# Kernel tuning notes

Measured on AMD Instinct MI355X. Metric: run time of the kernel, lower is better.

The kernel has to match this reference:

```python
import jax, jax.numpy as jnp
import numpy as np

N = 50000
E = 800000
D_IN, D_HID, D_OUT = 256, 512, 256
LN_EPS = 1e-5


def setup_inputs() -> dict:
    key = jax.random.key(0)
    ks = jax.random.split(key, 8)
    return {
        "v": jax.random.normal(ks[0], (N, D_IN), dtype=jnp.float32),
        "edge_weight": jax.random.uniform(ks[1], (E,), dtype=jnp.float32),
        "epsilon": jnp.zeros((1, 1), dtype=jnp.float32),
        "w1": jax.random.normal(ks[2], (D_HID, D_IN), dtype=jnp.float32) * (1.0 / np.sqrt(D_IN)),
        "b1": jnp.zeros((D_HID,), dtype=jnp.float32),
        "g1": jnp.ones((D_HID,), dtype=jnp.float32),
        "beta1": jnp.zeros((D_HID,), dtype=jnp.float32),
        "w2": jax.random.normal(ks[3], (D_OUT, D_HID), dtype=jnp.float32) * (1.0 / np.sqrt(D_HID)),
        "b2": jnp.zeros((D_OUT,), dtype=jnp.float32),
        "g2": jnp.ones((D_OUT,), dtype=jnp.float32),
        "beta2": jnp.zeros((D_OUT,), dtype=jnp.float32),
        "src": jax.random.randint(ks[4], (E,), 0, N, dtype=jnp.int32),
        "dst": jax.random.randint(ks[5], (E,), 0, N, dtype=jnp.int32),
    }


def _layer_norm(x, g, b):
    mu = jnp.mean(x, axis=-1, keepdims=True)
    var = jnp.mean(jnp.square(x - mu), axis=-1, keepdims=True)
    return (x - mu) * jax.lax.rsqrt(var + LN_EPS) * g + b


def reference(v, edge_weight, epsilon, w1, b1, g1, beta1, w2, b2, g2, beta2, src, dst):
    # sparse adjacency aggregation: agg[dst] += w * v[src]   (torch.sparse.mm(a, v))
    msgs = v[src] * edge_weight[:, None]            # [E, D_IN]
    agg = jax.ops.segment_sum(msgs, dst, num_segments=v.shape[0])  # [N, D_IN]
    h = agg + epsilon * v                            # epsilon residual
    # MLP: Linear -> LayerNorm -> ReLU  (x2)
    h = jax.nn.relu(_layer_norm(h @ w1.T + b1, g1, beta1))
    h = jax.nn.relu(_layer_norm(h @ w2.T + b2, g2, beta2))
    return h
```

## Files before the change

### kernel.cpp

```cpp
#include <hip/hip_runtime.h>

#define D_IN 256
#define D_HID 512
#define D_OUT 256
#define LN_EPS 1e-5f
#define SCAN_B 512

typedef __attribute__((ext_vector_type(8))) short bf16x8;
typedef __attribute__((ext_vector_type(4))) float f32x4;

__device__ __forceinline__ ushort f2bf(float x) {
    union { float f; unsigned u; } c; c.f = x;
    unsigned r = c.u + 0x7FFFu + ((c.u >> 16) & 1u);
    return (ushort)(r >> 16);
}
__device__ __forceinline__ float bf2f(unsigned b) {
    union { unsigned u; float f; } c; c.u = b << 16;
    return c.f;
}

__global__ void prep_kernel(const float* __restrict__ v, const float* __restrict__ w1,
                            const float* __restrict__ w2, ushort* __restrict__ vb,
                            ushort* __restrict__ w1p, ushort* __restrict__ w2p,
                            const int* __restrict__ dst, int* __restrict__ rank,
                            int* __restrict__ cnt, int n4v, int E,
                            int bv, int bw) {
    int b = blockIdx.x, t = threadIdx.x;
    if (b < bv) {
        int i = b * 256 + t;
        if (i < n4v) {
            float4 x = ((const float4*)v)[i];
            ((ushort4*)vb)[i] = make_ushort4(f2bf(x.x), f2bf(x.y), f2bf(x.z), f2bf(x.w));
        }
    } else if (b < bv + bw) {
        int j = (b - bv) * 256 + t;
        if (j < 32768) {
            int f = j * 4;
            int row = f >> 8, col = f & 255;
            float4 x = ((const float4*)w1)[j];
            int rb = row >> 4, fr = row & 15;
            int kb32 = col >> 5, q = (col & 31) >> 3, e = col & 7;
            int chunk = (kb32 * 32 + rb) * 64 + q * 16 + fr;
            *(ushort4*)(w1p + chunk * 8 + e) =
                make_ushort4(f2bf(x.x), f2bf(x.y), f2bf(x.z), f2bf(x.w));
        } else {
            int k = j - 32768;
            int f = k * 4;
            int row = f >> 9, col = f & 511;
            float4 x = ((const float4*)w2)[k];
            int rb = row >> 4, fr = row & 15;
            int kb32 = col >> 5, q = (col & 31) >> 3, e = col & 7;
            int chunk = (kb32 * 16 + rb) * 64 + q * 16 + fr;
            *(ushort4*)(w2p + chunk * 8 + e) =
                make_ushort4(f2bf(x.x), f2bf(x.y), f2bf(x.z), f2bf(x.w));
        }
    } else {
        int e = (b - bv - bw) * 256 + t;
        if (e < E) rank[e] = atomicAdd(&cnt[dst[e]], 1);
    }
}

__global__ __launch_bounds__(SCAN_B) void scan1_kernel(const int* __restrict__ cnt,
                                                       int* __restrict__ offs,
                                                       int* __restrict__ bsum, int n) {
    __shared__ int s[SCAN_B];
    int i = blockIdx.x * SCAN_B + threadIdx.x;
    int x = (i < n) ? cnt[i] : 0;
    s[threadIdx.x] = x;
    __syncthreads();
    for (int o = 1; o < SCAN_B; o <<= 1) {
        int t = (threadIdx.x >= (unsigned)o) ? s[threadIdx.x - o] : 0;
        __syncthreads();
        s[threadIdx.x] += t;
        __syncthreads();
    }
    if (i < n) offs[i] = s[threadIdx.x] - x;
    if (threadIdx.x == SCAN_B - 1) bsum[blockIdx.x] = s[threadIdx.x];
}

__global__ __launch_bounds__(SCAN_B) void scan3_kernel(int* __restrict__ offs,
                                                       const int* __restrict__ bsum,
                                                       int n, int E, int nb) {
    __shared__ int s[SCAN_B];
    int t = threadIdx.x;
    s[t] = (t < nb && t < (int)blockIdx.x) ? bsum[t] : 0;
    __syncthreads();
    for (int o = SCAN_B / 2; o > 0; o >>= 1) {
        if (t < o) s[t] += s[t + o];
        __syncthreads();
    }
    int base = s[0];
    int i = blockIdx.x * SCAN_B + t;
    if (i < n) offs[i] += base;
    if (i == 0) offs[n] = E;
}

__global__ void fill_kernel(const int* __restrict__ src, const int* __restrict__ dst,
                            const float* __restrict__ ew, const int* __restrict__ rank,
                            const int* __restrict__ offs,
                            int2* __restrict__ perm, int E) {
    int e = blockIdx.x * 256 + threadIdx.x;
    if (e >= E) return;
    int p = offs[dst[e]] + rank[e];
    perm[p] = make_int2(src[e], __float_as_int(ew[e]));
}

__global__ __launch_bounds__(256) void aggregate_kernel(
    const ushort* __restrict__ vb, const float* __restrict__ eps_p,
    const int* __restrict__ offs, const int2* __restrict__ perm,
    ushort* __restrict__ aggb, int N) {
    int node = blockIdx.x * 4 + (threadIdx.x >> 6);
    if (node >= N) return;
    int lane = threadIdx.x & 63;
    int beg = offs[node], end = offs[node + 1];
    float a0 = 0.f, a1 = 0.f, a2 = 0.f, a3 = 0.f;
    float c0 = 0.f, c1 = 0.f, c2 = 0.f, c3 = 0.f;

    int i = beg;
    for (; i + 8 <= end; i += 8) {
        int2 p0 = perm[i + 0], p1 = perm[i + 1], p2 = perm[i + 2], p3 = perm[i + 3];
        int2 p4 = perm[i + 4], p5 = perm[i + 5], p6 = perm[i + 6], p7 = perm[i + 7];
        float w0 = __int_as_float(p0.y), w1 = __int_as_float(p1.y);
        float w2 = __int_as_float(p2.y), w3 = __int_as_float(p3.y);
        float w4 = __int_as_float(p4.y), w5 = __int_as_float(p5.y);
        float w6 = __int_as_float(p6.y), w7 = __int_as_float(p7.y);
        ushort4 r0 = ((const ushort4*)(vb + (size_t)p0.x * D_IN))[lane];
        ushort4 r1 = ((const ushort4*)(vb + (size_t)p1.x * D_IN))[lane];
        ushort4 r2 = ((const ushort4*)(vb + (size_t)p2.x * D_IN))[lane];
        ushort4 r3 = ((const ushort4*)(vb + (size_t)p3.x * D_IN))[lane];
        ushort4 r4 = ((const ushort4*)(vb + (size_t)p4.x * D_IN))[lane];
        ushort4 r5 = ((const ushort4*)(vb + (size_t)p5.x * D_IN))[lane];
        ushort4 r6 = ((const ushort4*)(vb + (size_t)p6.x * D_IN))[lane];
        ushort4 r7 = ((const ushort4*)(vb + (size_t)p7.x * D_IN))[lane];
        a0 += w0 * bf2f(r0.x) + w1 * bf2f(r1.x) + w2 * bf2f(r2.x) + w3 * bf2f(r3.x);
        a1 += w0 * bf2f(r0.y) + w1 * bf2f(r1.y) + w2 * bf2f(r2.y) + w3 * bf2f(r3.y);
        a2 += w0 * bf2f(r0.z) + w1 * bf2f(r1.z) + w2 * bf2f(r2.z) + w3 * bf2f(r3.z);
        a3 += w0 * bf2f(r0.w) + w1 * bf2f(r1.w) + w2 * bf2f(r2.w) + w3 * bf2f(r3.w);
        c0 += w4 * bf2f(r4.x) + w5 * bf2f(r5.x) + w6 * bf2f(r6.x) + w7 * bf2f(r7.x);
        c1 += w4 * bf2f(r4.y) + w5 * bf2f(r5.y) + w6 * bf2f(r6.y) + w7 * bf2f(r7.y);
        c2 += w4 * bf2f(r4.z) + w5 * bf2f(r5.z) + w6 * bf2f(r6.z) + w7 * bf2f(r7.z);
        c3 += w4 * bf2f(r4.w) + w5 * bf2f(r5.w) + w6 * bf2f(r6.w) + w7 * bf2f(r7.w);
    }
    for (; i + 4 <= end; i += 4) {
        int2 p0 = perm[i + 0], p1 = perm[i + 1], p2 = perm[i + 2], p3 = perm[i + 3];
        float w0 = __int_as_float(p0.y), w1 = __int_as_float(p1.y);
        float w2 = __int_as_float(p2.y), w3 = __int_as_float(p3.y);
        ushort4 r0 = ((const ushort4*)(vb + (size_t)p0.x * D_IN))[lane];
        ushort4 r1 = ((const ushort4*)(vb + (size_t)p1.x * D_IN))[lane];
        ushort4 r2 = ((const ushort4*)(vb + (size_t)p2.x * D_IN))[lane];
        ushort4 r3 = ((const ushort4*)(vb + (size_t)p3.x * D_IN))[lane];
        a0 += w0 * bf2f(r0.x) + w1 * bf2f(r1.x) + w2 * bf2f(r2.x) + w3 * bf2f(r3.x);
        a1 += w0 * bf2f(r0.y) + w1 * bf2f(r1.y) + w2 * bf2f(r2.y) + w3 * bf2f(r3.y);
        a2 += w0 * bf2f(r0.z) + w1 * bf2f(r1.z) + w2 * bf2f(r2.z) + w3 * bf2f(r3.z);
        a3 += w0 * bf2f(r0.w) + w1 * bf2f(r1.w) + w2 * bf2f(r2.w) + w3 * bf2f(r3.w);
    }
    for (; i < end; ++i) {
        int2 p = perm[i];
        float w = __int_as_float(p.y);
        ushort4 r = ((const ushort4*)(vb + (size_t)p.x * D_IN))[lane];
        a0 += w * bf2f(r.x); a1 += w * bf2f(r.y);
        a2 += w * bf2f(r.z); a3 += w * bf2f(r.w);
    }
    a0 += c0; a1 += c1; a2 += c2; a3 += c3;
    float eps = eps_p[0];
    ushort4 m = ((const ushort4*)(vb + (size_t)node * D_IN))[lane];
    a0 += eps * bf2f(m.x); a1 += eps * bf2f(m.y);
    a2 += eps * bf2f(m.z); a3 += eps * bf2f(m.w);
    ((ushort4*)(aggb + (size_t)node * D_IN))[lane] =
        make_ushort4(f2bf(a0), f2bf(a1), f2bf(a2), f2bf(a3));
}

#define HS_IDX(row, col) ((row) * 512 + ((col) ^ (((row) & 7) << 3)))
#define AT_IDX(row, col) ((row) * 256 + ((col) ^ (((row) & 7) << 3)))

__global__ __launch_bounds__(256, 2) void mlp_kernel(
    const ushort* __restrict__ A, const ushort* __restrict__ w1p,
    const ushort* __restrict__ w2p,
    const float* __restrict__ b1, const float* __restrict__ g1, const float* __restrict__ be1,
    const float* __restrict__ b2, const float* __restrict__ g2, const float* __restrict__ be2,
    float* __restrict__ out, int N) {
    __shared__ ushort hs[32768];
    __shared__ float redf[640];

    int t = threadIdx.x;
    int w = t >> 6, lane = t & 63;
    int row0 = blockIdx.x * 64;
    int fr = lane & 15, q = lane >> 4, kb = q * 8;

    #pragma unroll
    for (int j = 0; j < 8; ++j) {
        int p = (w * 8 + j) * 64 + lane;
        int row = p >> 5, cbs = p & 31;
        int colblk = cbs ^ (row & 7);
        int ar = row0 + row; if (ar > N - 1) ar = N - 1;
        const ushort* gp = A + (size_t)ar * D_IN + colblk * 8;
        __builtin_amdgcn_global_load_lds(
            (const __attribute__((address_space(1))) void*)gp,
            (__attribute__((address_space(3))) void*)(&hs[(w * 8 + j) * 512]),
            16, 0, 0);
    }

    bf16x8 bfb[2][8];
    #pragma unroll
    for (int c = 0; c < 8; ++c)
        bfb[0][c] = *(const bf16x8*)(w1p + (size_t)((0 * 32 + w * 8 + c) * 64 + lane) * 8);

    __syncthreads();

    f32x4 acc[4][8];
    #pragma unroll
    for (int m = 0; m < 4; ++m)
        #pragma unroll
        for (int c = 0; c < 8; ++c) {
            f32x4 z = {0.f, 0.f, 0.f, 0.f};
            acc[m][c] = z;
        }

    #pragma unroll
    for (int ks = 0; ks < 8; ++ks) {
        const int cur = ks & 1, nxt = cur ^ 1;
        if (ks < 7) {
            #pragma unroll
            for (int c = 0; c < 8; ++c)
                bfb[nxt][c] = *(const bf16x8*)(w1p +
                    (size_t)(((ks + 1) * 32 + w * 8 + c) * 64 + lane) * 8);
        }
        bf16x8 af[4];
        #pragma unroll
        for (int m = 0; m < 4; ++m)
            af[m] = *(const bf16x8*)&hs[AT_IDX(m * 16 + fr, ks * 32 + kb)];
        #pragma unroll
        for (int m = 0; m < 4; ++m)
            #pragma unroll
            for (int c = 0; c < 8; ++c)
                acc[m][c] = __builtin_amdgcn_mfma_f32_16x16x32_bf16(af[m], bfb[cur][c], acc[m][c], 0, 0, 0);
    }

    {
        float bi[8], gg[8], bb[8];
        #pragma unroll
        for (int c = 0; c < 8; ++c) {
            int col = w * 128 + c * 16 + fr;
            bi[c] = b1[col]; gg[c] = g1[col]; bb[c] = be1[col];
        }
        #pragma unroll
        for (int m = 0; m < 4; ++m) {
            #pragma unroll
            for (int r = 0; r < 4; ++r) {
                float s = 0.f, sq = 0.f;
                #pragma unroll
                for (int c = 0; c < 8; ++c) {
                    float x = acc[m][c][r] + bi[c];
                    acc[m][c][r] = x;
                    s += x; sq += x * x;
                }
                #pragma unroll
                for (int o = 1; o < 16; o <<= 1) {
                    s  += __shfl_xor(s, o, 64);
                    sq += __shfl_xor(sq, o, 64);
                }
                if (fr == 0) {
                    int row = m * 16 + q * 4 + r;
                    redf[row * 4 + w]       = s;
                    redf[256 + row * 4 + w] = sq;
                }
            }
        }
        __syncthreads();
        if (t < 64) {
            float s  = redf[t * 4 + 0] + redf[t * 4 + 1] + redf[t * 4 + 2] + redf[t * 4 + 3];
            float sq = redf[256 + t * 4 + 0] + redf[256 + t * 4 + 1] +
                       redf[256 + t * 4 + 2] + redf[256 + t * 4 + 3];
            float mu = s / (float)D_HID;
            float var = sq / (float)D_HID - mu * mu;
            redf[512 + t] = mu;
            redf[576 + t] = rsqrtf(var + LN_EPS);
        }
        __syncthreads();
        #pragma unroll
        for (int m = 0; m < 4; ++m) {
            #pragma unroll
            for (int r = 0; r < 4; ++r) {
                int row = m * 16 + q * 4 + r;
                float mu = redf[512 + row], rs = redf[576 + row];
                #pragma unroll
                for (int c = 0; c < 8; ++c) {
                    int col = w * 128 + c * 16 + fr;
                    float y = (acc[m][c][r] - mu) * rs * gg[c] + bb[c];
                    hs[HS_IDX(row, col)] = f2bf(fmaxf(y, 0.f));
                }
            }
        }
    }

    bf16x8 bf2b[2][4][2];
    #pragma unroll
    for (int c = 0; c < 4; ++c)
        #pragma unroll
        for (int h = 0; h < 2; ++h)
            bf2b[0][c][h] = *(const bf16x8*)(w2p +
                (size_t)(((0 + h) * 16 + w * 4 + c) * 64 + lane) * 8);

    __syncthreads();

    f32x4 acc2[4][4];
    #pragma unroll
    for (int m = 0; m < 4; ++m)
        #pragma unroll
        for (int c = 0; c < 4; ++c) {
            f32x4 z = {0.f, 0.f, 0.f, 0.f};
            acc2[m][c] = z;
        }

    #pragma unroll
    for (int s = 0; s < 8; ++s) {
        const int cur = s & 1, nxt = cur ^ 1;
        if (s < 7) {
            #pragma unroll
            for (int c = 0; c < 4; ++c)
                #pragma unroll
                for (int h = 0; h < 2; ++h)
                    bf2b[nxt][c][h] = *(const bf16x8*)(w2p +
                        (size_t)(((2 * (s + 1) + h) * 16 + w * 4 + c) * 64 + lane) * 8);
        }
        bf16x8 af2[4][2];
        #pragma unroll
        for (int m = 0; m < 4; ++m)
            #pragma unroll
            for (int h = 0; h < 2; ++h)
                af2[m][h] = *(const bf16x8*)&hs[HS_IDX(m * 16 + fr, s * 64 + h * 32 + kb)];
        #pragma unroll
        for (int m = 0; m < 4; ++m)
            #pragma unroll
            for (int c = 0; c < 4; ++c)
                #pragma unroll
                for (int h = 0; h < 2; ++h)
                    acc2[m][c] = __builtin_amdgcn_mfma_f32_16x16x32_bf16(af2[m][h], bf2b[cur][c][h], acc2[m][c], 0, 0, 0);
    }

    {
        float bi[4], gg[4], bb[4];
        #pragma unroll
        for (int c = 0; c < 4; ++c) {
            int col = w * 64 + c * 16 + fr;
            bi[c] = b2[col]; gg[c] = g2[col]; bb[c] = be2[col];
        }
        #pragma unroll
        for (int m = 0; m < 4; ++m) {
            #pragma unroll
            for (int r = 0; r < 4; ++r) {
                float s = 0.f, sq = 0.f;
                #pragma unroll
                for (int c = 0; c < 4; ++c) {
                    float x = acc2[m][c][r] + bi[c];
                    acc2[m][c][r] = x;
                    s += x; sq += x * x;
                }
                #pragma unroll
                for (int o = 1; o < 16; o <<= 1) {
                    s  += __shfl_xor(s, o, 64);
                    sq += __shfl_xor(sq, o, 64);
                }
                if (fr == 0) {
                    int row = m * 16 + q * 4 + r;
                    redf[row * 4 + w]       = s;
                    redf[256 + row * 4 + w] = sq;
                }
            }
        }
        __syncthreads();
        if (t < 64) {
            float s  = redf[t * 4 + 0] + redf[t * 4 + 1] + redf[t * 4 + 2] + redf[t * 4 + 3];
            float sq = redf[256 + t * 4 + 0] + redf[256 + t * 4 + 1] +
                       redf[256 + t * 4 + 2] + redf[256 + t * 4 + 3];
            float mu = s / (float)D_OUT;
            float var = sq / (float)D_OUT - mu * mu;
            redf[512 + t] = mu;
            redf[576 + t] = rsqrtf(var + LN_EPS);
        }
        __syncthreads();
        #pragma unroll
        for (int m = 0; m < 4; ++m) {
            #pragma unroll
            for (int r = 0; r < 4; ++r) {
                int row = m * 16 + q * 4 + r;
                int grow = row0 + row;
                if (grow >= N) continue;
                float mu = redf[512 + row], rs = redf[576 + row];
                #pragma unroll
                for (int c = 0; c < 4; ++c) {
                    int col = w * 64 + c * 16 + fr;
                    float y = (acc2[m][c][r] - mu) * rs * gg[c] + bb[c];
                    out[(size_t)grow * D_OUT + col] = fmaxf(y, 0.f);
                }
            }
        }
    }
}

extern "C" void kernel_launch(void* const* d_in, const int* in_sizes, int n_in,
                              void* d_out, int out_size, void* d_ws, size_t ws_size,
                              hipStream_t stream) {
    const float* v     = (const float*)d_in[0];
    const float* ew    = (const float*)d_in[1];
    const float* eps   = (const float*)d_in[2];
    const float* w1    = (const float*)d_in[3];
    const float* b1    = (const float*)d_in[4];
    const float* g1    = (const float*)d_in[5];
    const float* beta1 = (const float*)d_in[6];
    const float* w2    = (const float*)d_in[7];
    const float* b2    = (const float*)d_in[8];
    const float* g2    = (const float*)d_in[9];
    const float* beta2 = (const float*)d_in[10];
    const int*   src   = (const int*)d_in[11];
    const int*   dst   = (const int*)d_in[12];

    int N = in_sizes[0] / D_IN;
    int E = in_sizes[1];

    float* out = (float*)d_out;

    char* ws = (char*)d_ws;
    size_t off = 0;
    ushort* vb   = (ushort*)(ws + off); off += (size_t)N * D_IN * 2;
    ushort* aggb = (ushort*)(ws + off); off += (size_t)N * D_IN * 2;
    ushort* w1p  = (ushort*)(ws + off); off += (size_t)D_HID * D_IN * 2;
    ushort* w2p  = (ushort*)(ws + off); off += (size_t)D_OUT * D_HID * 2;
    int* offs     = (int*)(ws + off); off += (size_t)(N + 256) * 4;
    int* cnt      = (int*)(ws + off); off += (size_t)(N + 256) * 4;
    int* bsum     = (int*)(ws + off); off += 1024;
    int* rank     = (int*)(ws + off); off += (size_t)E * 4;
    int2* perm    = (int2*)(ws + off); off += (size_t)E * 8;

    int nb = (N + SCAN_B - 1) / SCAN_B;
    int n4v = N * (D_IN / 4);
    int bv = (n4v + 255) / 256;
    int bw = 256;
    int be = (E + 255) / 256;

    hipMemsetAsync(cnt, 0, (size_t)N * 4, stream);

    prep_kernel<<<bv + bw + be, 256, 0, stream>>>(v, w1, w2, vb, w1p, w2p,
                                                  dst, rank, cnt, n4v, E, bv, bw);

    scan1_kernel<<<nb, SCAN_B, 0, stream>>>(cnt, offs, bsum, N);
    scan3_kernel<<<nb, SCAN_B, 0, stream>>>(offs, bsum, N, E, nb);

    fill_kernel<<<be, 256, 0, stream>>>(src, dst, ew, rank, offs, perm, E);

    aggregate_kernel<<<(N + 3) / 4, 256, 0, stream>>>(vb, eps, offs, perm, aggb, N);

    int mblocks = (N + 63) / 64;
    mlp_kernel<<<mblocks, 256, 0, stream>>>(aggb, w1p, w2p,
                                            b1, g1, beta1, b2, g2, beta2, out, N);
}
```

Measured before the change: 294.7 us.

## Fuse preprocessing, scan, fill and aggregation into one persistent kernel with grid barriers

Replaces the prep, two scan, fill and aggregate launches with a single persistent kernel of fixed grid size that uses atomic-counter grid barriers between phases. The scan is restructured into 256-element chunks plus a single-block scan of chunk sums, and the base offsets are applied lazily when reading. The aim is to remove several kernel launch gaps and tail effects. In exchange, grid-stride loops run at lower occupancy, and the software barriers rely on all 960 blocks being co-resident, which risks deadlock if they are not.

```diff
diff --git a/kernel.cpp b/kernel.cpp
--- a/kernel.cpp
+++ b/kernel.cpp
@@ -4,7 +4,8 @@
 #define D_HID 512
 #define D_OUT 256
 #define LN_EPS 1e-5f
-#define SCAN_B 512
+#define NBLK 960
+#define NTHR (NBLK * 256)
 
 typedef __attribute__((ext_vector_type(8))) short bf16x8;
 typedef __attribute__((ext_vector_type(4))) float f32x4;
@@ -19,21 +20,35 @@
     return c.f;
 }
 
-__global__ void prep_kernel(const float* __restrict__ v, const float* __restrict__ w1,
-                            const float* __restrict__ w2, ushort* __restrict__ vb,
-                            ushort* __restrict__ w1p, ushort* __restrict__ w2p,
-                            const int* __restrict__ dst, int* __restrict__ rank,
-                            int* __restrict__ cnt, int n4v, int E,
-                            int bv, int bw) {
-    int b = blockIdx.x, t = threadIdx.x;
-    if (b < bv) {
-        int i = b * 256 + t;
-        if (i < n4v) {
-            float4 x = ((const float4*)v)[i];
-            ((ushort4*)vb)[i] = make_ushort4(f2bf(x.x), f2bf(x.y), f2bf(x.z), f2bf(x.w));
-        }
-    } else if (b < bv + bw) {
-        int j = (b - bv) * 256 + t;
+__device__ __forceinline__ void gbar(int* bar, int k) {
+    __threadfence();
+    __syncthreads();
+    if (threadIdx.x == 0) {
+        atomicAdd(&bar[k], 1);
+        while (atomicAdd(&bar[k], 0) < NBLK) __builtin_amdgcn_s_sleep(2);
+    }
+    __syncthreads();
+    __threadfence();
+}
+
+__global__ __launch_bounds__(256, 4) void mega_kernel(
+    const float* __restrict__ v, const float* __restrict__ w1,
+    const float* __restrict__ w2, ushort* __restrict__ vb,
+    ushort* __restrict__ w1p, ushort* __restrict__ w2p,
+    const int* __restrict__ src, const int* __restrict__ dst,
+    const float* __restrict__ ew, const float* __restrict__ eps_p,
+    int* __restrict__ rank, int* __restrict__ cnt, int* __restrict__ bar,
+    int* __restrict__ offs, int* __restrict__ bsum, int2* __restrict__ perm,
+    ushort* __restrict__ aggb, int N, int E, int n4v, int nch) {
+    __shared__ int s[256];
+    int t = threadIdx.x, b = blockIdx.x;
+    int tid = b * 256 + t;
+
+    for (int i = tid; i < n4v; i += NTHR) {
+        float4 x = ((const float4*)v)[i];
+        ((ushort4*)vb)[i] = make_ushort4(f2bf(x.x), f2bf(x.y), f2bf(x.z), f2bf(x.w));
+    }
+    for (int j = tid; j < 65536; j += NTHR) {
         if (j < 32768) {
             int f = j * 4;
             int row = f >> 8, col = f & 255;
@@ -54,120 +69,113 @@
             *(ushort4*)(w2p + chunk * 8 + e) =
                 make_ushort4(f2bf(x.x), f2bf(x.y), f2bf(x.z), f2bf(x.w));
         }
-    } else {
-        int e = (b - bv - bw) * 256 + t;
-        if (e < E) rank[e] = atomicAdd(&cnt[dst[e]], 1);
-    }
-}
-
-__global__ __launch_bounds__(SCAN_B) void scan1_kernel(const int* __restrict__ cnt,
-                                                       int* __restrict__ offs,
-                                                       int* __restrict__ bsum, int n) {
-    __shared__ int s[SCAN_B];
-    int i = blockIdx.x * SCAN_B + threadIdx.x;
-    int x = (i < n) ? cnt[i] : 0;
-    s[threadIdx.x] = x;
-    __syncthreads();
-    for (int o = 1; o < SCAN_B; o <<= 1) {
-        int t = (threadIdx.x >= (unsigned)o) ? s[threadIdx.x - o] : 0;
-        __syncthreads();
-        s[threadIdx.x] += t;
-        __syncthreads();
-    }
-    if (i < n) offs[i] = s[threadIdx.x] - x;
-    if (threadIdx.x == SCAN_B - 1) bsum[blockIdx.x] = s[threadIdx.x];
-}
-
-__global__ __launch_bounds__(SCAN_B) void scan3_kernel(int* __restrict__ offs,
-                                                       const int* __restrict__ bsum,
-                                                       int n, int E, int nb) {
-    __shared__ int s[SCAN_B];
-    int t = threadIdx.x;
-    s[t] = (t < nb && t < (int)blockIdx.x) ? bsum[t] : 0;
-    __syncthreads();
-    for (int o = SCAN_B / 2; o > 0; o >>= 1) {
-        if (t < o) s[t] += s[t + o];
-        __syncthreads();
-    }
-    int base = s[0];
-    int i = blockIdx.x * SCAN_B + t;
-    if (i < n) offs[i] += base;
-    if (i == 0) offs[n] = E;
-}
-
-__global__ void fill_kernel(const int* __restrict__ src, const int* __restrict__ dst,
-                            const float* __restrict__ ew, const int* __restrict__ rank,
-                            const int* __restrict__ offs,
-                            int2* __restrict__ perm, int E) {
-    int e = blockIdx.x * 256 + threadIdx.x;
-    if (e >= E) return;
-    int p = offs[dst[e]] + rank[e];
-    perm[p] = make_int2(src[e], __float_as_int(ew[e]));
-}
-
-__global__ __launch_bounds__(256) void aggregate_kernel(
-    const ushort* __restrict__ vb, const float* __restrict__ eps_p,
-    const int* __restrict__ offs, const int2* __restrict__ perm,
-    ushort* __restrict__ aggb, int N) {
-    int node = blockIdx.x * 4 + (threadIdx.x >> 6);
-    if (node >= N) return;
-    int lane = threadIdx.x & 63;
-    int beg = offs[node], end = offs[node + 1];
-    float a0 = 0.f, a1 = 0.f, a2 = 0.f, a3 = 0.f;
-    float c0 = 0.f, c1 = 0.f, c2 = 0.f, c3 = 0.f;
-
-    int i = beg;
-    for (; i + 8 <= end; i += 8) {
-        int2 p0 = perm[i + 0], p1 = perm[i + 1], p2 = perm[i + 2], p3 = perm[i + 3];
-        int2 p4 = perm[i + 4], p5 = perm[i + 5], p6 = perm[i + 6], p7 = perm[i + 7];
-        float w0 = __int_as_float(p0.y), w1 = __int_as_float(p1.y);
-        float w2 = __int_as_float(p2.y), w3 = __int_as_float(p3.y);
-        float w4 = __int_as_float(p4.y), w5 = __int_as_float(p5.y);
-        float w6 = __int_as_float(p6.y), w7 = __int_as_float(p7.y);
-        ushort4 r0 = ((const ushort4*)(vb + (size_t)p0.x * D_IN))[lane];
-        ushort4 r1 = ((const ushort4*)(vb + (size_t)p1.x * D_IN))[lane];
-        ushort4 r2 = ((const ushort4*)(vb + (size_t)p2.x * D_IN))[lane];
-        ushort4 r3 = ((const ushort4*)(vb + (size_t)p3.x * D_IN))[lane];
-        ushort4 r4 = ((const ushort4*)(vb + (size_t)p4.x * D_IN))[lane];
-        ushort4 r5 = ((const ushort4*)(vb + (size_t)p5.x * D_IN))[lane];
-        ushort4 r6 = ((const ushort4*)(vb + (size_t)p6.x * D_IN))[lane];
-        ushort4 r7 = ((const ushort4*)(vb + (size_t)p7.x * D_IN))[lane];
-        a0 += w0 * bf2f(r0.x) + w1 * bf2f(r1.x) + w2 * bf2f(r2.x) + w3 * bf2f(r3.x);
-        a1 += w0 * bf2f(r0.y) + w1 * bf2f(r1.y) + w2 * bf2f(r2.y) + w3 * bf2f(r3.y);
-        a2 += w0 * bf2f(r0.z) + w1 * bf2f(r1.z) + w2 * bf2f(r2.z) + w3 * bf2f(r3.z);
-        a3 += w0 * bf2f(r0.w) + w1 * bf2f(r1.w) + w2 * bf2f(r2.w) + w3 * bf2f(r3.w);
-        c0 += w4 * bf2f(r4.x) + w5 * bf2f(r5.x) + w6 * bf2f(r6.x) + w7 * bf2f(r7.x);
-        c1 += w4 * bf2f(r4.y) + w5 * bf2f(r5.y) + w6 * bf2f(r6.y) + w7 * bf2f(r7.y);
-        c2 += w4 * bf2f(r4.z) + w5 * bf2f(r5.z) + w6 * bf2f(r6.z) + w7 * bf2f(r7.z);
-        c3 += w4 * bf2f(r4.w) + w5 * bf2f(r5.w) + w6 * bf2f(r6.w) + w7 * bf2f(r7.w);
-    }
-    for (; i + 4 <= end; i += 4) {
-        int2 p0 = perm[i + 0], p1 = perm[i + 1], p2 = perm[i + 2], p3 = perm[i + 3];
-        float w0 = __int_as_float(p0.y), w1 = __int_as_float(p1.y);
-        float w2 = __int_as_float(p2.y), w3 = __int_as_float(p3.y);
-        ushort4 r0 = ((const ushort4*)(vb + (size_t)p0.x * D_IN))[lane];
-        ushort4 r1 = ((const ushort4*)(vb + (size_t)p1.x * D_IN))[lane];
-        ushort4 r2 = ((const ushort4*)(vb + (size_t)p2.x * D_IN))[lane];
-        ushort4 r3 = ((const ushort4*)(vb + (size_t)p3.x * D_IN))[lane];
-        a0 += w0 * bf2f(r0.x) + w1 * bf2f(r1.x) + w2 * bf2f(r2.x) + w3 * bf2f(r3.x);
-        a1 += w0 * bf2f(r0.y) + w1 * bf2f(r1.y) + w2 * bf2f(r2.y) + w3 * bf2f(r3.y);
-        a2 += w0 * bf2f(r0.z) + w1 * bf2f(r1.z) + w2 * bf2f(r2.z) + w3 * bf2f(r3.z);
-        a3 += w0 * bf2f(r0.w) + w1 * bf2f(r1.w) + w2 * bf2f(r2.w) + w3 * bf2f(r3.w);
-    }
-    for (; i < end; ++i) {
-        int2 p = perm[i];
-        float w = __int_as_float(p.y);
-        ushort4 r = ((const ushort4*)(vb + (size_t)p.x * D_IN))[lane];
-        a0 += w * bf2f(r.x); a1 += w * bf2f(r.y);
-        a2 += w * bf2f(r.z); a3 += w * bf2f(r.w);
-    }
-    a0 += c0; a1 += c1; a2 += c2; a3 += c3;
-    float eps = eps_p[0];
-    ushort4 m = ((const ushort4*)(vb + (size_t)node * D_IN))[lane];
-    a0 += eps * bf2f(m.x); a1 += eps * bf2f(m.y);
-    a2 += eps * bf2f(m.z); a3 += eps * bf2f(m.w);
-    ((ushort4*)(aggb + (size_t)node * D_IN))[lane] =
-        make_ushort4(f2bf(a0), f2bf(a1), f2bf(a2), f2bf(a3));
+    }
+    for (int e = tid; e < E; e += NTHR)
+        rank[e] = atomicAdd(&cnt[dst[e]], 1);
+
+    gbar(bar, 0);
+
+    if (b < nch) {
+        int i = b * 256 + t;
+        int x = cnt[i];
+        s[t] = x;
+        __syncthreads();
+        for (int o = 1; o < 256; o <<= 1) {
+            int u = (t >= o) ? s[t - o] : 0;
+            __syncthreads();
+            s[t] += u;
+            __syncthreads();
+        }
+        offs[i] = s[t] - x;
+        if (t == 255) bsum[b] = s[t];
+    }
+    gbar(bar, 1);
+
+    if (b == 0) {
+        int x = (t < nch) ? bsum[t] : 0;
+        s[t] = x;
+        __syncthreads();
+        for (int o = 1; o < 256; o <<= 1) {
+            int u = (t >= o) ? s[t - o] : 0;
+            __syncthreads();
+            s[t] += u;
+            __syncthreads();
+        }
+        bsum[t] = s[t] - x;
+    }
+    gbar(bar, 2);
+
+    for (int e = tid; e < E; e += NTHR) {
+        int d = dst[e];
+        int p = bsum[d >> 8] + offs[d] + rank[e];
+        perm[p] = make_int2(src[e], __float_as_int(ew[e]));
+    }
+    gbar(bar, 3);
+
+    {
+        const float eps = eps_p[0];
+        int lane = t & 63;
+        int wid = b * 4 + (t >> 6);
+        for (int node = wid; node < N; node += NBLK * 4) {
+            int beg = bsum[node >> 8] + offs[node];
+            int m = node + 1;
+            int end = (m < nch * 256) ? (bsum[m >> 8] + offs[m]) : E;
+            float a0 = 0.f, a1 = 0.f, a2 = 0.f, a3 = 0.f;
+            float c0 = 0.f, c1 = 0.f, c2 = 0.f, c3 = 0.f;
+
+            int i = beg;
+            for (; i + 8 <= end; i += 8) {
+                int2 p0 = perm[i + 0], p1 = perm[i + 1], p2 = perm[i + 2], p3 = perm[i + 3];
+                int2 p4 = perm[i + 4], p5 = perm[i + 5], p6 = perm[i + 6], p7 = perm[i + 7];
+                float w0 = __int_as_float(p0.y), w1_ = __int_as_float(p1.y);
+                float w2_ = __int_as_float(p2.y), w3 = __int_as_float(p3.y);
+                float w4 = __int_as_float(p4.y), w5 = __int_as_float(p5.y);
+                float w6 = __int_as_float(p6.y), w7 = __int_as_float(p7.y);
+                ushort4 r0 = ((const ushort4*)(vb + (size_t)p0.x * D_IN))[lane];
+                ushort4 r1 = ((const ushort4*)(vb + (size_t)p1.x * D_IN))[lane];
+                ushort4 r2 = ((const ushort4*)(vb + (size_t)p2.x * D_IN))[lane];
+                ushort4 r3 = ((const ushort4*)(vb + (size_t)p3.x * D_IN))[lane];
+                ushort4 r4 = ((const ushort4*)(vb + (size_t)p4.x * D_IN))[lane];
+                ushort4 r5 = ((const ushort4*)(vb + (size_t)p5.x * D_IN))[lane];
+                ushort4 r6 = ((const ushort4*)(vb + (size_t)p6.x * D_IN))[lane];
+                ushort4 r7 = ((const ushort4*)(vb + (size_t)p7.x * D_IN))[lane];
+                a0 += w0 * bf2f(r0.x) + w1_ * bf2f(r1.x) + w2_ * bf2f(r2.x) + w3 * bf2f(r3.x);
+                a1 += w0 * bf2f(r0.y) + w1_ * bf2f(r1.y) + w2_ * bf2f(r2.y) + w3 * bf2f(r3.y);
+                a2 += w0 * bf2f(r0.z) + w1_ * bf2f(r1.z) + w2_ * bf2f(r2.z) + w3 * bf2f(r3.z);
+                a3 += w0 * bf2f(r0.w) + w1_ * bf2f(r1.w) + w2_ * bf2f(r2.w) + w3 * bf2f(r3.w);
+                c0 += w4 * bf2f(r4.x) + w5 * bf2f(r5.x) + w6 * bf2f(r6.x) + w7 * bf2f(r7.x);
+                c1 += w4 * bf2f(r4.y) + w5 * bf2f(r5.y) + w6 * bf2f(r6.y) + w7 * bf2f(r7.y);
+                c2 += w4 * bf2f(r4.z) + w5 * bf2f(r5.z) + w6 * bf2f(r6.z) + w7 * bf2f(r7.z);
+                c3 += w4 * bf2f(r4.w) + w5 * bf2f(r5.w) + w6 * bf2f(r6.w) + w7 * bf2f(r7.w);
+            }
+            for (; i + 4 <= end; i += 4) {
+                int2 p0 = perm[i + 0], p1 = perm[i + 1], p2 = perm[i + 2], p3 = perm[i + 3];
+                float w0 = __int_as_float(p0.y), w1_ = __int_as_float(p1.y);
+                float w2_ = __int_as_float(p2.y), w3 = __int_as_float(p3.y);
+                ushort4 r0 = ((const ushort4*)(vb + (size_t)p0.x * D_IN))[lane];
+                ushort4 r1 = ((const ushort4*)(vb + (size_t)p1.x * D_IN))[lane];
+                ushort4 r2 = ((const ushort4*)(vb + (size_t)p2.x * D_IN))[lane];
+                ushort4 r3 = ((const ushort4*)(vb + (size_t)p3.x * D_IN))[lane];
+                a0 += w0 * bf2f(r0.x) + w1_ * bf2f(r1.x) + w2_ * bf2f(r2.x) + w3 * bf2f(r3.x);
+                a1 += w0 * bf2f(r0.y) + w1_ * bf2f(r1.y) + w2_ * bf2f(r2.y) + w3 * bf2f(r3.y);
+                a2 += w0 * bf2f(r0.z) + w1_ * bf2f(r1.z) + w2_ * bf2f(r2.z) + w3 * bf2f(r3.z);
+                a3 += w0 * bf2f(r0.w) + w1_ * bf2f(r1.w) + w2_ * bf2f(r2.w) + w3 * bf2f(r3.w);
+            }
+            for (; i < end; ++i) {
+                int2 p = perm[i];
+                float we = __int_as_float(p.y);
+                ushort4 rr = ((const ushort4*)(vb + (size_t)p.x * D_IN))[lane];
+                a0 += we * bf2f(rr.x); a1 += we * bf2f(rr.y);
+                a2 += we * bf2f(rr.z); a3 += we * bf2f(rr.w);
+            }
+            a0 += c0; a1 += c1; a2 += c2; a3 += c3;
+            ushort4 mv = ((const ushort4*)(vb + (size_t)node * D_IN))[lane];
+            a0 += eps * bf2f(mv.x); a1 += eps * bf2f(mv.y);
+            a2 += eps * bf2f(mv.z); a3 += eps * bf2f(mv.w);
+            ((ushort4*)(aggb + (size_t)node * D_IN))[lane] =
+                make_ushort4(f2bf(a0), f2bf(a1), f2bf(a2), f2bf(a3));
+        }
+    }
 }
 
 #define HS_IDX(row, col) ((row) * 512 + ((col) ^ (((row) & 7) << 3)))
@@ -203,7 +211,7 @@
     bf16x8 bfb[2][8];
     #pragma unroll
     for (int c = 0; c < 8; ++c)
-        bfb[0][c] = *(const bf16x8*)(w1p + (size_t)((0 * 32 + w * 8 + c) * 64 + lane) * 8);
+        bfb[0][c] = *(const bf16x8*)(w1p + (size_t)((w * 8 + c) * 64 + lane) * 8);
 
     __syncthreads();
 
@@ -313,22 +321,22 @@
         }
 
     #pragma unroll
-    for (int s = 0; s < 8; ++s) {
-        const int cur = s & 1, nxt = cur ^ 1;
-        if (s < 7) {
+    for (int s2 = 0; s2 < 8; ++s2) {
+        const int cur = s2 & 1, nxt = cur ^ 1;
+        if (s2 < 7) {
             #pragma unroll
             for (int c = 0; c < 4; ++c)
                 #pragma unroll
                 for (int h = 0; h < 2; ++h)
                     bf2b[nxt][c][h] = *(const bf16x8*)(w2p +
-                        (size_t)(((2 * (s + 1) + h) * 16 + w * 4 + c) * 64 + lane) * 8);
+                        (size_t)(((2 * (s2 + 1) + h) * 16 + w * 4 + c) * 64 + lane) * 8);
         }
         bf16x8 af2[4][2];
         #pragma unroll
         for (int m = 0; m < 4; ++m)
             #pragma unroll
             for (int h = 0; h < 2; ++h)
-                af2[m][h] = *(const bf16x8*)&hs[HS_IDX(m * 16 + fr, s * 64 + h * 32 + kb)];
+                af2[m][h] = *(const bf16x8*)&hs[HS_IDX(m * 16 + fr, s2 * 64 + h * 32 + kb)];
         #pragma unroll
         for (int m = 0; m < 4; ++m)
             #pragma unroll
@@ -428,27 +436,20 @@
     ushort* w2p  = (ushort*)(ws + off); off += (size_t)D_OUT * D_HID * 2;
     int* offs     = (int*)(ws + off); off += (size_t)(N + 256) * 4;
     int* cnt      = (int*)(ws + off); off += (size_t)(N + 256) * 4;
+    int* bar      = (int*)(ws + off); off += 64 * 4;
     int* bsum     = (int*)(ws + off); off += 1024;
     int* rank     = (int*)(ws + off); off += (size_t)E * 4;
     int2* perm    = (int2*)(ws + off); off += (size_t)E * 8;
 
-    int nb = (N + SCAN_B - 1) / SCAN_B;
     int n4v = N * (D_IN / 4);
-    int bv = (n4v + 255) / 256;
-    int bw = 256;
-    int be = (E + 255) / 256;
-
-    hipMemsetAsync(cnt, 0, (size_t)N * 4, stream);
-
-    prep_kernel<<<bv + bw + be, 256, 0, stream>>>(v, w1, w2, vb, w1p, w2p,
-                                                  dst, rank, cnt, n4v, E, bv, bw);
-
-    scan1_kernel<<<nb, SCAN_B, 0, stream>>>(cnt, offs, bsum, N);
-    scan3_kernel<<<nb, SCAN_B, 0, stream>>>(offs, bsum, N, E, nb);
-
-    fill_kernel<<<be, 256, 0, stream>>>(src, dst, ew, rank, offs, perm, E);
-
-    aggregate_kernel<<<(N + 3) / 4, 256, 0, stream>>>(vb, eps, offs, perm, aggb, N);
+    int nch = (N + 255) / 256;
+
+    hipMemsetAsync(cnt, 0, ((size_t)(N + 256) + 64) * 4, stream);
+
+    mega_kernel<<<NBLK, 256, 0, stream>>>(v, w1, w2, vb, w1p, w2p,
+                                          src, dst, ew, eps,
+                                          rank, cnt, bar, offs, bsum, perm,
+                                          aggb, N, E, n4v, nch);
 
     int mblocks = (N + 63) / 64;
     mlp_kernel<<<mblocks, 256, 0, stream>>>(aggb, w1p, w2p,
```

Measured after the change: 1.117 ms. 3.79x slower.

## Split MLP kernel work across 8 waves per block instead of 4

Applied to the files above, without the earlier changes.

The fused MLP kernel now launches 512 threads (8 waves) per 64-row block, with each wave covering half as many output columns in both GEMMs. Per-wave accumulator and weight-fragment registers are halved, and the LayerNorm reductions are widened to combine partials from 8 waves. The aim is more resident waves per CU to hide memory and MFMA latency. In exchange, every wave still reloads the full A fragments from LDS, so LDS read traffic per block doubles, and launch bounds of 512 threads with 4 blocks may cap registers tightly.

```diff
diff --git a/kernel.cpp b/kernel.cpp
--- a/kernel.cpp
+++ b/kernel.cpp
@@ -173,14 +173,14 @@
 #define HS_IDX(row, col) ((row) * 512 + ((col) ^ (((row) & 7) << 3)))
 #define AT_IDX(row, col) ((row) * 256 + ((col) ^ (((row) & 7) << 3)))
 
-__global__ __launch_bounds__(256, 2) void mlp_kernel(
+__global__ __launch_bounds__(512, 4) void mlp_kernel(
     const ushort* __restrict__ A, const ushort* __restrict__ w1p,
     const ushort* __restrict__ w2p,
     const float* __restrict__ b1, const float* __restrict__ g1, const float* __restrict__ be1,
     const float* __restrict__ b2, const float* __restrict__ g2, const float* __restrict__ be2,
     float* __restrict__ out, int N) {
     __shared__ ushort hs[32768];
-    __shared__ float redf[640];
+    __shared__ float redf[1152];
 
     int t = threadIdx.x;
     int w = t >> 6, lane = t & 63;
@@ -188,30 +188,30 @@
     int fr = lane & 15, q = lane >> 4, kb = q * 8;
 
     #pragma unroll
-    for (int j = 0; j < 8; ++j) {
-        int p = (w * 8 + j) * 64 + lane;
+    for (int j = 0; j < 4; ++j) {
+        int p = (w * 4 + j) * 64 + lane;
         int row = p >> 5, cbs = p & 31;
         int colblk = cbs ^ (row & 7);
         int ar = row0 + row; if (ar > N - 1) ar = N - 1;
         const ushort* gp = A + (size_t)ar * D_IN + colblk * 8;
         __builtin_amdgcn_global_load_lds(
             (const __attribute__((address_space(1))) void*)gp,
-            (__attribute__((address_space(3))) void*)(&hs[(w * 8 + j) * 512]),
+            (__attribute__((address_space(3))) void*)(&hs[(w * 4 + j) * 512]),
             16, 0, 0);
     }
 
-    bf16x8 bfb[2][8];
-    #pragma unroll
-    for (int c = 0; c < 8; ++c)
-        bfb[0][c] = *(const bf16x8*)(w1p + (size_t)((0 * 32 + w * 8 + c) * 64 + lane) * 8);
+    bf16x8 bfb[2][4];
+    #pragma unroll
+    for (int c = 0; c < 4; ++c)
+        bfb[0][c] = *(const bf16x8*)(w1p + (size_t)(((0) * 32 + w * 4 + c) * 64 + lane) * 8);
 
     __syncthreads();
 
-    f32x4 acc[4][8];
+    f32x4 acc[4][4];
     #pragma unroll
     for (int m = 0; m < 4; ++m)
         #pragma unroll
-        for (int c = 0; c < 8; ++c) {
+        for (int c = 0; c < 4; ++c) {
             f32x4 z = {0.f, 0.f, 0.f, 0.f};
             acc[m][c] = z;
         }
@@ -221,9 +221,9 @@
         const int cur = ks & 1, nxt = cur ^ 1;
         if (ks < 7) {
             #pragma unroll
-            for (int c = 0; c < 8; ++c)
+            for (int c = 0; c < 4; ++c)
                 bfb[nxt][c] = *(const bf16x8*)(w1p +
-                    (size_t)(((ks + 1) * 32 + w * 8 + c) * 64 + lane) * 8);
+                    (size_t)(((ks + 1) * 32 + w * 4 + c) * 64 + lane) * 8);
         }
         bf16x8 af[4];
         #pragma unroll
@@ -232,15 +232,15 @@
         #pragma unroll
         for (int m = 0; m < 4; ++m)
             #pragma unroll
-            for (int c = 0; c < 8; ++c)
+            for (int c = 0; c < 4; ++c)
                 acc[m][c] = __builtin_amdgcn_mfma_f32_16x16x32_bf16(af[m], bfb[cur][c], acc[m][c], 0, 0, 0);
     }
 
     {
-        float bi[8], gg[8], bb[8];
-        #pragma unroll
-        for (int c = 0; c < 8; ++c) {
-            int col = w * 128 + c * 16 + fr;
+        float bi[4], gg[4], bb[4];
+        #pragma unroll
+        for (int c = 0; c < 4; ++c) {
+            int col = w * 64 + c * 16 + fr;
             bi[c] = b1[col]; gg[c] = g1[col]; bb[c] = be1[col];
         }
         #pragma unroll
@@ -249,7 +249,7 @@
             for (int r = 0; r < 4; ++r) {
                 float s = 0.f, sq = 0.f;
                 #pragma unroll
-                for (int c = 0; c < 8; ++c) {
+                for (int c = 0; c < 4; ++c) {
                     float x = acc[m][c][r] + bi[c];
                     acc[m][c][r] = x;
                     s += x; sq += x * x;
@@ -261,20 +261,23 @@
                 }
                 if (fr == 0) {
                     int row = m * 16 + q * 4 + r;
-                    redf[row * 4 + w]       = s;
-                    redf[256 + row * 4 + w] = sq;
+                    redf[row * 8 + w]       = s;
+                    redf[512 + row * 8 + w] = sq;
                 }
             }
         }
         __syncthreads();
         if (t < 64) {
-            float s  = redf[t * 4 + 0] + redf[t * 4 + 1] + redf[t * 4 + 2] + redf[t * 4 + 3];
-            float sq = redf[256 + t * 4 + 0] + redf[256 + t * 4 + 1] +
-                       redf[256 + t * 4 + 2] + redf[256 + t * 4 + 3];
+            float s = 0.f, sq = 0.f;
+            #pragma unroll
+            for (int k = 0; k < 8; ++k) {
+                s  += redf[t * 8 + k];
+                sq += redf[512 + t * 8 + k];
+            }
             float mu = s / (float)D_HID;
             float var = sq / (float)D_HID - mu * mu;
-            redf[512 + t] = mu;
-            redf[576 + t] = rsqrtf(var + LN_EPS);
+            redf[1024 + t] = mu;
+            redf[1088 + t] = rsqrtf(var + LN_EPS);
         }
         __syncthreads();
         #pragma unroll
@@ -282,10 +285,10 @@
             #pragma unroll
             for (int r = 0; r < 4; ++r) {
                 int row = m * 16 + q * 4 + r;
-                float mu = redf[512 + row], rs = redf[576 + row];
-                #pragma unroll
-                for (int c = 0; c < 8; ++c) {
-                    int col = w * 128 + c * 16 + fr;
+                float mu = redf[1024 + row], rs = redf[1088 + row];
+                #pragma unroll
+                for (int c = 0; c < 4; ++c) {
+                    int col = w * 64 + c * 16 + fr;
                     float y = (acc[m][c][r] - mu) * rs * gg[c] + bb[c];
                     hs[HS_IDX(row, col)] = f2bf(fmaxf(y, 0.f));
                 }
@@ -293,56 +296,56 @@
         }
     }
 
-    bf16x8 bf2b[2][4][2];
-    #pragma unroll
-    for (int c = 0; c < 4; ++c)
+    bf16x8 bf2b[2][2][2];
+    #pragma unroll
+    for (int c = 0; c < 2; ++c)
         #pragma unroll
         for (int h = 0; h < 2; ++h)
             bf2b[0][c][h] = *(const bf16x8*)(w2p +
-                (size_t)(((0 + h) * 16 + w * 4 + c) * 64 + lane) * 8);
+                (size_t)(((0 + h) * 16 + w * 2 + c) * 64 + lane) * 8);
 
     __syncthreads();
 
-    f32x4 acc2[4][4];
+    f32x4 acc2[4][2];
     #pragma unroll
     for (int m = 0; m < 4; ++m)
         #pragma unroll
-        for (int c = 0; c < 4; ++c) {
+        for (int c = 0; c < 2; ++c) {
             f32x4 z = {0.f, 0.f, 0.f, 0.f};
             acc2[m][c] = z;
         }
 
     #pragma unroll
-    for (int s = 0; s < 8; ++s) {
-        const int cur = s & 1, nxt = cur ^ 1;
-        if (s < 7) {
-            #pragma unroll
-            for (int c = 0; c < 4; ++c)
+    for (int s2 = 0; s2 < 8; ++s2) {
+        const int cur = s2 & 1, nxt = cur ^ 1;
+        if (s2 < 7) {
+            #pragma unroll
+            for (int c = 0; c < 2; ++c)
                 #pragma unroll
                 for (int h = 0; h < 2; ++h)
                     bf2b[nxt][c][h] = *(const bf16x8*)(w2p +
-                        (size_t)(((2 * (s + 1) + h) * 16 + w * 4 + c) * 64 + lane) * 8);
+                        (size_t)(((2 * (s2 + 1) + h) * 16 + w * 2 + c) * 64 + lane) * 8);
         }
         bf16x8 af2[4][2];
         #pragma unroll
         for (int m = 0; m < 4; ++m)
             #pragma unroll
             for (int h = 0; h < 2; ++h)
-                af2[m][h] = *(const bf16x8*)&hs[HS_IDX(m * 16 + fr, s * 64 + h * 32 + kb)];
+                af2[m][h] = *(const bf16x8*)&hs[HS_IDX(m * 16 + fr, s2 * 64 + h * 32 + kb)];
         #pragma unroll
         for (int m = 0; m < 4; ++m)
             #pragma unroll
-            for (int c = 0; c < 4; ++c)
+            for (int c = 0; c < 2; ++c)
                 #pragma unroll
                 for (int h = 0; h < 2; ++h)
                     acc2[m][c] = __builtin_amdgcn_mfma_f32_16x16x32_bf16(af2[m][h], bf2b[cur][c][h], acc2[m][c], 0, 0, 0);
     }
 
     {
-        float bi[4], gg[4], bb[4];
-        #pragma unroll
-        for (int c = 0; c < 4; ++c) {
-            int col = w * 64 + c * 16 + fr;
+        float bi[2], gg[2], bb[2];
+        #pragma unroll
+        for (int c = 0; c < 2; ++c) {
+            int col = w * 32 + c * 16 + fr;
             bi[c] = b2[col]; gg[c] = g2[col]; bb[c] = be2[col];
         }
         #pragma unroll
@@ -351,7 +354,7 @@
             for (int r = 0; r < 4; ++r) {
                 float s = 0.f, sq = 0.f;
                 #pragma unroll
-                for (int c = 0; c < 4; ++c) {
+                for (int c = 0; c < 2; ++c) {
                     float x = acc2[m][c][r] + bi[c];
                     acc2[m][c][r] = x;
                     s += x; sq += x * x;
@@ -363,20 +366,23 @@
                 }
                 if (fr == 0) {
                     int row = m * 16 + q * 4 + r;
-                    redf[row * 4 + w]       = s;
-                    redf[256 + row * 4 + w] = sq;
+                    redf[row * 8 + w]       = s;
+                    redf[512 + row * 8 + w] = sq;
                 }
             }
         }
         __syncthreads();
         if (t < 64) {
-            float s  = redf[t * 4 + 0] + redf[t * 4 + 1] + redf[t * 4 + 2] + redf[t * 4 + 3];
-            float sq = redf[256 + t * 4 + 0] + redf[256 + t * 4 + 1] +
-                       redf[256 + t * 4 + 2] + redf[256 + t * 4 + 3];
+            float s = 0.f, sq = 0.f;
+            #pragma unroll
+            for (int k = 0; k < 8; ++k) {
+                s  += redf[t * 8 + k];
+                sq += redf[512 + t * 8 + k];
+            }
             float mu = s / (float)D_OUT;
             float var = sq / (float)D_OUT - mu * mu;
-            redf[512 + t] = mu;
-            redf[576 + t] = rsqrtf(var + LN_EPS);
+            redf[1024 + t] = mu;
+            redf[1088 + t] = rsqrtf(var + LN_EPS);
         }
         __syncthreads();
         #pragma unroll
@@ -386,10 +392,10 @@
                 int row = m * 16 + q * 4 + r;
                 int grow = row0 + row;
                 if (grow >= N) continue;
-                float mu = redf[512 + row], rs = redf[576 + row];
-                #pragma unroll
-                for (int c = 0; c < 4; ++c) {
-                    int col = w * 64 + c * 16 + fr;
+                float mu = redf[1024 + row], rs = redf[1088 + row];
+                #pragma unroll
+                for (int c = 0; c < 2; ++c) {
+                    int col = w * 32 + c * 16 + fr;
                     float y = (acc2[m][c][r] - mu) * rs * gg[c] + bb[c];
                     out[(size_t)grow * D_OUT + col] = fmaxf(y, 0.f);
                 }
@@ -432,11 +438,11 @@
     int* rank     = (int*)(ws + off); off += (size_t)E * 4;
     int2* perm    = (int2*)(ws + off); off += (size_t)E * 8;
 
-    int nb = (N + SCAN_B - 1) / SCAN_B;
     int n4v = N * (D_IN / 4);
     int bv = (n4v + 255) / 256;
     int bw = 256;
     int be = (E + 255) / 256;
+    int nb = (N + SCAN_B - 1) / SCAN_B;
 
     hipMemsetAsync(cnt, 0, (size_t)N * 4, stream);
 
@@ -451,6 +457,6 @@
     aggregate_kernel<<<(N + 3) / 4, 256, 0, stream>>>(vb, eps, offs, perm, aggb, N);
 
     int mblocks = (N + 63) / 64;
-    mlp_kernel<<<mblocks, 256, 0, stream>>>(aggb, w1p, w2p,
+    mlp_kernel<<<mblocks, 512, 0, stream>>>(aggb, w1p, w2p,
                                             b1, g1, beta1, b2, g2, beta2, out, N);
 }
```

Measured after the change: 304.6 us. +3.3%, slower.
